# Optimization experiments

Measured on AMD Instinct MI355X. Metric: run time of the kernel, lower is better.

Reference implementation:

```python
import jax, jax.numpy as jnp
import numpy as np

D_MODEL = 2048
N_HEADS = 16
D_K = D_MODEL // N_HEADS


def setup_inputs() -> dict:
    key = jax.random.key(0)
    ks = jax.random.split(key, 9)
    s = 1.0 / np.sqrt(D_MODEL)
    def lin(k):
        kw, kb = jax.random.split(k)
        W = jax.random.uniform(kw, (D_MODEL, D_MODEL), jnp.float32, -s, s)
        b = jax.random.uniform(kb, (D_MODEL,), jnp.float32, -s, s)
        return W, b
    Wq, bq = lin(ks[0])
    Wk, bk = lin(ks[1])
    Wv, bv = lin(ks[2])
    Wo, bo = lin(ks[3])
    x = jax.random.normal(ks[4], (2, 2048, D_MODEL), jnp.float32)
    return {"x": x, "Wq": Wq, "bq": bq, "Wk": Wk, "bk": bk,
            "Wv": Wv, "bv": bv, "Wo": Wo, "bo": bo}


def _mha(x, Wq, bq, Wk, bk, Wv, bv, Wo, bo):
    B, S, _ = x.shape
    # Linear projections (torch Linear: x @ W.T + b), split into heads: b s (h d) -> b h s d
    def proj(W, b):
        y = jnp.einsum('bsm,nm->bsn', x, W) + b
        return y.reshape(B, S, N_HEADS, D_K).transpose(0, 2, 1, 3)
    q = proj(Wq, bq)
    k = proj(Wk, bk)
    v = proj(Wv, bv)
    scores = jnp.einsum('bhsd,bhtd->bhst', q, k) / jnp.sqrt(jnp.float32(D_K))
    causal = jnp.triu(jnp.ones((S, S), bool), k=1)  # True above diagonal -> masked
    scores = jnp.where(causal[None, None], -jnp.inf, scores)
    attn = jax.nn.softmax(scores, axis=-1)  # dropout p=0 (eval)
    out = jnp.einsum('bhst,bhtd->bhsd', attn, v)
    out = out.transpose(0, 2, 1, 3).reshape(B, S, D_MODEL)
    return jnp.einsum('bsm,nm->bsn', out, Wo) + bo


def reference(x, Wq, bq, Wk, bk, Wv, bv, Wo, bo):
    return _mha(x, Wq, bq, Wk, bk, Wv, bv, Wo, bo)
```

## Files before the change

kernel.cpp:

```cpp
#include <hip/hip_runtime.h>

typedef unsigned short u16;
typedef __attribute__((ext_vector_type(8))) short bf16x8;
typedef __attribute__((ext_vector_type(4))) float f32x4;
typedef __attribute__((ext_vector_type(4))) unsigned short u16x4;

__device__ __forceinline__ u16 f2bf(float f) {
  union { float f; unsigned u; } v; v.f = f;
  return (u16)((v.u + 0x7FFFu + ((v.u >> 16) & 1u)) >> 16);
}

__device__ __forceinline__ void gload16(const u16* g, u16* l) {
  __builtin_amdgcn_global_load_lds((const __attribute__((address_space(1))) void*)g,
                                   (__attribute__((address_space(3))) void*)l, 16, 0, 0);
}

__global__ __launch_bounds__(256) void k_f2bf5(
    const float* __restrict__ i0, const float* __restrict__ i1, const float* __restrict__ i2,
    const float* __restrict__ i3, const float* __restrict__ i4,
    u16* o0, u16* o1, u16* o2, u16* o3, u16* o4, int n4x, int n4w) {
  const int seg = blockIdx.y;
  const float* in = (seg == 0) ? i0 : (seg == 1) ? i1 : (seg == 2) ? i2 : (seg == 3) ? i3 : i4;
  u16* out = (seg == 0) ? o0 : (seg == 1) ? o1 : (seg == 2) ? o2 : (seg == 3) ? o3 : o4;
  const int n4 = (seg == 0) ? n4x : n4w;
  int i = blockIdx.x * 256 + threadIdx.x;
  const int stride = gridDim.x * 256;
  for (; i < n4; i += stride) {
    const float4 v = ((const float4*)in)[i];
    u16x4 o;
    o.x = f2bf(v.x); o.y = f2bf(v.y); o.z = f2bf(v.z); o.w = f2bf(v.w);
    ((u16x4*)out)[i] = o;
  }
}

template <int OUT_F32>
__global__ __launch_bounds__(256) void k_gemm_bias(
    const u16* __restrict__ A,
    const u16* __restrict__ Bt0, const u16* __restrict__ Bt1, const u16* __restrict__ Bt2,
    const float* __restrict__ b0, const float* __restrict__ b1, const float* __restrict__ b2,
    u16* __restrict__ C0, u16* __restrict__ C1, u16* __restrict__ C2,
    float* __restrict__ Cf, int M, int N, int K)
{
  const int z = blockIdx.z;
  const u16* Bt = (z == 0) ? Bt0 : (z == 1) ? Bt1 : Bt2;
  const float* bias = (z == 0) ? b0 : (z == 1) ? b1 : b2;
  u16* Cb = (z == 0) ? C0 : (z == 1) ? C1 : C2;

  __shared__ u16 As[128 * 64];
  __shared__ u16 Bs[128 * 64];
  const int tid = threadIdx.x;
  const int lane = tid & 63;
  const int wid = tid >> 6;
  const int fr = lane & 15;
  const int fg = lane >> 4;
  const int wr = wid >> 1, wc = wid & 1;
  const long row0 = (long)blockIdx.x * 128;
  const long col0 = (long)blockIdx.y * 128;

  f32x4 acc[4][4] = {};

  for (int k0 = 0; k0 < K; k0 += 64) {
    __syncthreads();
#pragma unroll
    for (int i = 0; i < 4; ++i) {
      const int chunk = (wid * 4 + i) * 64 + lane;
      const int r = chunk >> 3;
      const int c = (chunk & 7) << 3;
      gload16(A + (row0 + r) * (long)K + k0 + c, &As[(wid * 4 + i) * 512]);
      gload16(Bt + (col0 + r) * (long)K + k0 + c, &Bs[(wid * 4 + i) * 512]);
    }
    __syncthreads();

#pragma unroll
    for (int kc = 0; kc < 2; ++kc) {
      bf16x8 a[4], b[4];
#pragma unroll
      for (int i = 0; i < 4; ++i)
        a[i] = *(const bf16x8*)&As[(wr * 64 + i * 16 + fr) * 64 + kc * 32 + fg * 8];
#pragma unroll
      for (int j = 0; j < 4; ++j)
        b[j] = *(const bf16x8*)&Bs[(wc * 64 + j * 16 + fr) * 64 + kc * 32 + fg * 8];
#pragma unroll
      for (int i = 0; i < 4; ++i)
#pragma unroll
        for (int j = 0; j < 4; ++j)
          acc[i][j] = __builtin_amdgcn_mfma_f32_16x16x32_bf16(a[i], b[j], acc[i][j], 0, 0, 0);
    }
  }

#pragma unroll
  for (int j = 0; j < 4; ++j) {
    const long cN = col0 + wc * 64 + j * 16 + fr;
    const float bv = bias[cN];
#pragma unroll
    for (int i = 0; i < 4; ++i) {
      const long rM = row0 + wr * 64 + i * 16 + fg * 4;
#pragma unroll
      for (int reg = 0; reg < 4; ++reg) {
        const float v = acc[i][j][reg] + bv;
        if (OUT_F32) Cf[(rM + reg) * N + cN] = v;
        else         Cb[(rM + reg) * N + cN] = f2bf(v);
      }
    }
  }
}

__global__ __launch_bounds__(256) void k_transpose_v(const u16* __restrict__ V,
                                                     u16* __restrict__ Vt) {
  __shared__ u16 t[64][68];
  const int bh = blockIdx.z;
  const long s0 = (long)blockIdx.x * 64;
  const long d0 = (long)blockIdx.y * 64;
  const int tid = threadIdx.x;
  const long rowbase = (long)(bh >> 4) * 2048;
  const int hcol = (bh & 15) * 128;
#pragma unroll
  for (int i = 0; i < 4; ++i) {
    const int v = tid + i * 256;
    const int r = v >> 4, c4 = (v & 15) << 2;
    const u16x4 val = *(const u16x4*)&V[(rowbase + s0 + r) * 2048 + hcol + d0 + c4];
    *(u16x4*)&t[r][c4] = val;
  }
  __syncthreads();
#pragma unroll
  for (int i = 0; i < 4; ++i) {
    const int v = tid + i * 256;
    const int dr = v >> 4, s4 = (v & 15) << 2;
    u16x4 o;
    o.x = t[s4 + 0][dr]; o.y = t[s4 + 1][dr]; o.z = t[s4 + 2][dr]; o.w = t[s4 + 3][dr];
    *(u16x4*)&Vt[((long)bh * 128 + d0 + dr) * 2048 + s0 + s4] = o;
  }
}

__global__ __launch_bounds__(512) void k_flash_attn(
    const u16* __restrict__ Q, const u16* __restrict__ K, const u16* __restrict__ Vt,
    u16* __restrict__ O)
{
  __shared__ alignas(16) u16 Kt[2][8192];
  __shared__ alignas(16) u16 Vtt[2][8192];
  __shared__ alignas(16) u16 Plds[8][16][72];

  const int tid = threadIdx.x;
  const int lane = tid & 63, wid = tid >> 6;
  const int fr = lane & 15, fg = lane >> 4;

  const int L = blockIdx.x;
  const int bh = (L & 7) * 4 + ((L >> 3) & 3);
  const int bx = L >> 5;

  const long rowbase = (long)(bh >> 4) * 2048;
  const int hcol = (bh & 15) * 128;
  const u16* Kg = K + rowbase * 2048 + hcol;
  const u16* Vg = Vt + (long)bh * 128 * 2048;
  const float scale2 = 0.08838834764831845f * 1.44269504089f;

  int kR[2], kC[2], vR[2], vC[2];
#pragma unroll
  for (int i = 0; i < 2; ++i) {
    const int chunk = (wid * 2 + i) * 64 + lane;
    kR[i] = chunk >> 4;
    kC[i] = ((chunk & 15) ^ (kR[i] & 7)) << 3;
    vR[i] = chunk >> 3;
    vC[i] = ((chunk & 7) ^ (vR[i] & 7)) << 3;
  }

  const int sw = fr & 7;
  int kbase[4], vbase[2];
#pragma unroll
  for (int c = 0; c < 4; ++c) kbase[c] = fr * 128 + (((c * 4 + fg) ^ sw) << 3);
#pragma unroll
  for (int kc = 0; kc < 2; ++kc) vbase[kc] = fr * 64 + (((kc * 4 + fg) ^ sw) << 3);

  for (int pass = 0; pass < 2; ++pass) {
    const int qblk = pass ? (15 - bx) : bx;
    const int n = 2 * (qblk + 1);
    const int q_lo = qblk * 128 + wid * 16;

    bf16x8 qf[4];
#pragma unroll
    for (int c = 0; c < 4; ++c)
      qf[c] = *(const bf16x8*)&Q[(rowbase + q_lo + fr) * 2048 + hcol + c * 32 + fg * 8];

    f32x4 oacc[8] = {};
    float m_run[4], l_run[4];
#pragma unroll
    for (int r = 0; r < 4; ++r) { m_run[r] = -1e30f; l_run[r] = 0.0f; }

#pragma unroll
    for (int i = 0; i < 2; ++i) {
      gload16(Kg + (long)kR[i] * 2048 + kC[i], &Kt[0][(wid * 2 + i) * 512]);
      gload16(Vg + (long)vR[i] * 2048 + vC[i], &Vtt[0][(wid * 2 + i) * 512]);
    }

    int cur = 0;
    for (int j = 0; j < n; ++j) {
      if (j + 1 < n) {
        const long kv = (long)(j + 1) * 64;
#pragma unroll
        for (int i = 0; i < 2; ++i) {
          gload16(Kg + (kv + kR[i]) * 2048 + kC[i], &Kt[cur ^ 1][(wid * 2 + i) * 512]);
          gload16(Vg + (long)vR[i] * 2048 + kv + vC[i], &Vtt[cur ^ 1][(wid * 2 + i) * 512]);
        }
        asm volatile("s_waitcnt vmcnt(4)" ::: "memory");
      } else {
        asm volatile("s_waitcnt vmcnt(0)" ::: "memory");
      }
      __builtin_amdgcn_s_barrier();
      __builtin_amdgcn_sched_barrier(0);

      const int kvlo = j * 64;
      const bool skip = (kvlo >= q_lo + 16);
      if (!skip) {
        const bool needmask = (kvlo + 63 > q_lo);

        f32x4 st[4] = {};
        const u16* kt = Kt[cur];
#pragma unroll
        for (int t = 0; t < 4; ++t)
#pragma unroll
          for (int c = 0; c < 4; ++c) {
            const bf16x8 kf = *(const bf16x8*)&kt[kbase[c] + t * 2048];
            st[t] = __builtin_amdgcn_mfma_f32_16x16x32_bf16(qf[c], kf, st[t], 0, 0, 0);
          }

        float pmax[4] = {-1e30f, -1e30f, -1e30f, -1e30f};
        if (needmask) {
#pragma unroll
          for (int t = 0; t < 4; ++t) {
            const int kg = kvlo + t * 16 + fr;
#pragma unroll
            for (int r = 0; r < 4; ++r) {
              const int qg = q_lo + fg * 4 + r;
              const float v = (kg <= qg) ? st[t][r] * scale2 : -1e30f;
              st[t][r] = v;
              pmax[r] = fmaxf(pmax[r], v);
            }
          }
        } else {
#pragma unroll
          for (int t = 0; t < 4; ++t)
#pragma unroll
            for (int r = 0; r < 4; ++r) {
              const float v = st[t][r] * scale2;
              st[t][r] = v;
              pmax[r] = fmaxf(pmax[r], v);
            }
        }
#pragma unroll
        for (int d = 1; d < 16; d <<= 1)
#pragma unroll
          for (int r = 0; r < 4; ++r) pmax[r] = fmaxf(pmax[r], __shfl_xor(pmax[r], d));

        const int ok = (pmax[0] <= m_run[0] + 8.f) & (pmax[1] <= m_run[1] + 8.f) &
                       (pmax[2] <= m_run[2] + 8.f) & (pmax[3] <= m_run[3] + 8.f);
        if (!__all(ok)) {
#pragma unroll
          for (int r = 0; r < 4; ++r) {
            const float nm = fmaxf(m_run[r], pmax[r]);
            const float al = exp2f(m_run[r] - nm);
            l_run[r] *= al;
            m_run[r] = nm;
#pragma unroll
            for (int dt = 0; dt < 8; ++dt) oacc[dt][r] *= al;
          }
        }

        float lsum[4] = {0.f, 0.f, 0.f, 0.f};
#pragma unroll
        for (int t = 0; t < 4; ++t)
#pragma unroll
          for (int r = 0; r < 4; ++r) {
            const float p = exp2f(st[t][r] - m_run[r]);
            st[t][r] = p;
            lsum[r] += p;
          }
#pragma unroll
        for (int d = 1; d < 16; d <<= 1)
#pragma unroll
          for (int r = 0; r < 4; ++r) lsum[r] += __shfl_xor(lsum[r], d);
#pragma unroll
        for (int r = 0; r < 4; ++r) l_run[r] += lsum[r];

#pragma unroll
        for (int t = 0; t < 4; ++t)
#pragma unroll
          for (int r = 0; r < 4; ++r)
            Plds[wid][fg * 4 + r][t * 16 + fr] = f2bf(st[t][r]);
        asm volatile("s_waitcnt lgkmcnt(0)" ::: "memory");
        __builtin_amdgcn_sched_barrier(0);

        const u16* vt = Vtt[cur];
#pragma unroll
        for (int kc = 0; kc < 2; ++kc) {
          const bf16x8 pf = *(const bf16x8*)&Plds[wid][fr][kc * 32 + fg * 8];
#pragma unroll
          for (int dt = 0; dt < 8; ++dt) {
            const bf16x8 vf = *(const bf16x8*)&vt[vbase[kc] + dt * 1024];
            oacc[dt] = __builtin_amdgcn_mfma_f32_16x16x32_bf16(pf, vf, oacc[dt], 0, 0, 0);
          }
        }
      }

      asm volatile("" ::: "memory");
      __builtin_amdgcn_s_barrier();
      cur ^= 1;
    }

    float inv[4];
#pragma unroll
    for (int r = 0; r < 4; ++r) inv[r] = 1.0f / l_run[r];
#pragma unroll
    for (int dt = 0; dt < 8; ++dt)
#pragma unroll
      for (int r = 0; r < 4; ++r)
        O[(rowbase + q_lo + fg * 4 + r) * 2048 + hcol + dt * 16 + fr] = f2bf(oacc[dt][r] * inv[r]);
  }
}

extern "C" void kernel_launch(void* const* d_in, const int* in_sizes, int n_in,
                              void* d_out, int out_size, void* d_ws, size_t ws_size,
                              hipStream_t stream) {
  const float* x  = (const float*)d_in[0];
  const float* Wq = (const float*)d_in[1];
  const float* bq = (const float*)d_in[2];
  const float* Wk = (const float*)d_in[3];
  const float* bk = (const float*)d_in[4];
  const float* Wv = (const float*)d_in[5];
  const float* bv = (const float*)d_in[6];
  const float* Wo = (const float*)d_in[7];
  const float* bo = (const float*)d_in[8];
  float* out = (float*)d_out;

  const int M = 4096, N = 2048, Kd = 2048;
  char* ws = (char*)d_ws;
  const size_t SZ_X = 16777216;
  const size_t SZ_W = 8388608;
  u16* xb  = (u16*)(ws);
  u16* wqb = (u16*)(ws + SZ_X);
  u16* wkb = (u16*)(ws + SZ_X + 1 * SZ_W);
  u16* wvb = (u16*)(ws + SZ_X + 2 * SZ_W);
  u16* wob = (u16*)(ws + SZ_X + 3 * SZ_W);
  u16* Qb  = (u16*)(ws + 1 * SZ_X + 4 * SZ_W);
  u16* Kb  = (u16*)(ws + 2 * SZ_X + 4 * SZ_W);
  u16* Vb  = (u16*)(ws + 3 * SZ_X + 4 * SZ_W);
  u16* Vtb = (u16*)(ws + 4 * SZ_X + 4 * SZ_W);
  u16* Ob  = Vb;

  k_f2bf5<<<dim3(1024, 5), 256, 0, stream>>>(x, Wq, Wk, Wv, Wo,
                                             xb, wqb, wkb, wvb, wob,
                                             8388608 / 4, 4194304 / 4);

  k_gemm_bias<0><<<dim3(M / 128, N / 128, 3), 256, 0, stream>>>(
      xb, wqb, wkb, wvb, bq, bk, bv, Qb, Kb, Vb, nullptr, M, N, Kd);

  k_transpose_v<<<dim3(32, 2, 32), 256, 0, stream>>>(Vb, Vtb);

  k_flash_attn<<<256, 512, 0, stream>>>(Qb, Kb, Vtb, Ob);

  k_gemm_bias<1><<<dim3(M / 128, N / 128, 1), 256, 0, stream>>>(
      Ob, wob, wob, wob, bo, bo, bo, nullptr, nullptr, nullptr, out, M, N, Kd);
}
```

Baseline: 313.4 us.

## Replace projection GEMMs with 256x256 double-buffered swizzled LDS kernel

Replaces the 128x128 GEMM with a 512-thread kernel computing 256x256 tiles. It double-buffers LDS with global_load_lds prefetch of the next K tile and XOR-swizzles the LDS layout to avoid bank conflicts. It also interleaves MFMA phases with barriers and setprio, and remaps workgroups across XCDs for cache locality. The Q/K/V projections become one GEMM against the three contiguous weight matrices, and the bias/output pointer is picked per column segment. Larger tiles raise data reuse, at the cost of only 128 blocks for the output projection, which may underfill the GPU, plus heavy register and LDS use.

After: 322.9 us. 1.03x slower.

```diff
diff --git a/kernel.cpp b/kernel.cpp
--- a/kernel.cpp
+++ b/kernel.cpp
@@ -33,73 +33,122 @@
   }
 }
 
+#define LDA(AS, mh) do { _Pragma("unroll") \
+  for (int mi = 0; mi < 4; ++mi) { \
+    a[mi][0] = *(const bf16x8*)&(AS)[aBase + ((mh)*4+mi)*1024 + pc0]; \
+    a[mi][1] = *(const bf16x8*)&(AS)[aBase + ((mh)*4+mi)*1024 + pc1]; } } while(0)
+
+#define LDB(BS, nh) do { _Pragma("unroll") \
+  for (int ni = 0; ni < 2; ++ni) { \
+    b[nh][ni][0] = *(const bf16x8*)&(BS)[bBase + ((nh)*2+ni)*1024 + pc0]; \
+    b[nh][ni][1] = *(const bf16x8*)&(BS)[bBase + ((nh)*2+ni)*1024 + pc1]; } } while(0)
+
+#define MM(mh, nh) do { _Pragma("unroll") \
+  for (int mi = 0; mi < 4; ++mi) { _Pragma("unroll") \
+    for (int ni = 0; ni < 2; ++ni) { \
+      acc[(mh)*4+mi][(nh)*2+ni] = __builtin_amdgcn_mfma_f32_16x16x32_bf16( \
+          a[mi][0], b[nh][ni][0], acc[(mh)*4+mi][(nh)*2+ni], 0, 0, 0); \
+      acc[(mh)*4+mi][(nh)*2+ni] = __builtin_amdgcn_mfma_f32_16x16x32_bf16( \
+          a[mi][1], b[nh][ni][1], acc[(mh)*4+mi][(nh)*2+ni], 0, 0, 0); } } } while(0)
+
+#define MFMA_FENCE do { asm volatile("s_waitcnt lgkmcnt(0)" ::: "memory"); \
+  __builtin_amdgcn_sched_barrier(0); } while(0)
+
+#define KTILE(AS, BS, AN, BN_, tn) do { \
+   \
+  if ((tn) < NT) { const long kofs = (long)(tn) << 6; \
+    _Pragma("unroll") for (int i = 0; i < 4; ++i) { \
+      gload16(A  + (row0 + sRow[i]) * (long)K + kofs + sCol[i], &(AN)[(wid*4+i)*512]); \
+      gload16(Bt + (col0 + sRow[i]) * (long)K + kofs + sCol[i], &(BN_)[(wid*4+i)*512]); } } \
+  LDA(AS, 0); LDB(BS, 0); LDB(BS, 1); \
+  __builtin_amdgcn_s_barrier(); \
+  MFMA_FENCE; \
+  __builtin_amdgcn_s_setprio(1); MM(0, 0); __builtin_amdgcn_s_setprio(0); \
+  __builtin_amdgcn_s_barrier(); \
+   \
+  __builtin_amdgcn_s_setprio(1); MM(0, 1); __builtin_amdgcn_s_setprio(0); \
+  __builtin_amdgcn_s_barrier(); \
+   \
+  LDA(AS, 1); \
+  MFMA_FENCE; \
+  __builtin_amdgcn_s_setprio(1); MM(1, 0); __builtin_amdgcn_s_setprio(0); \
+  __builtin_amdgcn_s_barrier(); \
+   \
+  __builtin_amdgcn_s_setprio(1); MM(1, 1); __builtin_amdgcn_s_setprio(0); \
+  asm volatile("s_waitcnt vmcnt(0)" ::: "memory"); \
+  __builtin_amdgcn_s_barrier(); \
+} while(0)
+
 template <int OUT_F32>
-__global__ __launch_bounds__(256) void k_gemm_bias(
-    const u16* __restrict__ A,
-    const u16* __restrict__ Bt0, const u16* __restrict__ Bt1, const u16* __restrict__ Bt2,
+__global__ __launch_bounds__(512, 2) void k_gemm256(
+    const u16* __restrict__ A, const u16* __restrict__ Bt,
     const float* __restrict__ b0, const float* __restrict__ b1, const float* __restrict__ b2,
     u16* __restrict__ C0, u16* __restrict__ C1, u16* __restrict__ C2,
-    float* __restrict__ Cf, int M, int N, int K)
+    float* __restrict__ Cf, int NBM, int K)
 {
-  const int z = blockIdx.z;
-  const u16* Bt = (z == 0) ? Bt0 : (z == 1) ? Bt1 : Bt2;
-  const float* bias = (z == 0) ? b0 : (z == 1) ? b1 : b2;
-  u16* Cb = (z == 0) ? C0 : (z == 1) ? C1 : C2;
-
-  __shared__ u16 As[128 * 64];
-  __shared__ u16 Bs[128 * 64];
+  __shared__ alignas(16) u16 A0s[16384], B0s[16384], A1s[16384], B1s[16384];
+
   const int tid = threadIdx.x;
-  const int lane = tid & 63;
-  const int wid = tid >> 6;
-  const int fr = lane & 15;
-  const int fg = lane >> 4;
-  const int wr = wid >> 1, wc = wid & 1;
-  const long row0 = (long)blockIdx.x * 128;
-  const long col0 = (long)blockIdx.y * 128;
-
-  f32x4 acc[4][4] = {};
-
-  for (int k0 = 0; k0 < K; k0 += 64) {
-    __syncthreads();
-#pragma unroll
-    for (int i = 0; i < 4; ++i) {
-      const int chunk = (wid * 4 + i) * 64 + lane;
-      const int r = chunk >> 3;
-      const int c = (chunk & 7) << 3;
-      gload16(A + (row0 + r) * (long)K + k0 + c, &As[(wid * 4 + i) * 512]);
-      gload16(Bt + (col0 + r) * (long)K + k0 + c, &Bs[(wid * 4 + i) * 512]);
-    }
-    __syncthreads();
-
-#pragma unroll
-    for (int kc = 0; kc < 2; ++kc) {
-      bf16x8 a[4], b[4];
-#pragma unroll
-      for (int i = 0; i < 4; ++i)
-        a[i] = *(const bf16x8*)&As[(wr * 64 + i * 16 + fr) * 64 + kc * 32 + fg * 8];
-#pragma unroll
-      for (int j = 0; j < 4; ++j)
-        b[j] = *(const bf16x8*)&Bs[(wc * 64 + j * 16 + fr) * 64 + kc * 32 + fg * 8];
-#pragma unroll
-      for (int i = 0; i < 4; ++i)
-#pragma unroll
-        for (int j = 0; j < 4; ++j)
-          acc[i][j] = __builtin_amdgcn_mfma_f32_16x16x32_bf16(a[i], b[j], acc[i][j], 0, 0, 0);
-    }
-  }
-
-#pragma unroll
-  for (int j = 0; j < 4; ++j) {
-    const long cN = col0 + wc * 64 + j * 16 + fr;
-    const float bv = bias[cN];
-#pragma unroll
-    for (int i = 0; i < 4; ++i) {
-      const long rM = row0 + wr * 64 + i * 16 + fg * 4;
+  const int lane = tid & 63, wid = tid >> 6;
+  const int fr = lane & 15, fg = lane >> 4;
+  const int wr = wid >> 2, wc = wid & 3;
+
+  const int nblk = gridDim.x;
+  const int q = nblk >> 3, r = nblk & 7;
+  const int xcd = blockIdx.x & 7, lid = blockIdx.x >> 3;
+  const int wgid = (xcd < r ? xcd * (q + 1) : r * (q + 1) + (xcd - r) * q) + lid;
+  const int mb = wgid % NBM, nb = wgid / NBM;
+  const long row0 = (long)mb * 256;
+  const long col0 = (long)nb * 256;
+
+  int sRow[4], sCol[4];
+#pragma unroll
+  for (int i = 0; i < 4; ++i) {
+    const int s = (wid * 4 + i) * 64 + lane;
+    sRow[i] = s >> 3;
+    sCol[i] = ((s & 7) ^ ((s >> 3) & 7)) << 3;
+  }
+
+  const int sw = fr & 7;
+  const int aBase = (wr * 128 + fr) * 64;
+  const int bBase = (wc * 64 + fr) * 64;
+  const int pc0 = (fg ^ sw) << 3;
+  const int pc1 = ((4 + fg) ^ sw) << 3;
+
+  f32x4 acc[8][4] = {};
+  bf16x8 a[4][2], b[2][2][2];
+
+  const int NT = K >> 6;
+
+#pragma unroll
+  for (int i = 0; i < 4; ++i) {
+    gload16(A  + (row0 + sRow[i]) * (long)K + sCol[i], &A0s[(wid * 4 + i) * 512]);
+    gload16(Bt + (col0 + sRow[i]) * (long)K + sCol[i], &B0s[(wid * 4 + i) * 512]);
+  }
+  asm volatile("s_waitcnt vmcnt(0)" ::: "memory");
+  __builtin_amdgcn_s_barrier();
+
+  for (int t = 0; t < NT; t += 2) {
+    KTILE(A0s, B0s, A1s, B1s, t + 1);
+    KTILE(A1s, B1s, A0s, B0s, t + 2);
+  }
+
+  const int seg = (int)(col0 >> 11);
+  const long colL = col0 & 2047;
+  const float* bp = (seg == 0) ? b0 : (seg == 1) ? b1 : b2;
+  u16* Cb = (seg == 0) ? C0 : (seg == 1) ? C1 : C2;
+#pragma unroll
+  for (int n = 0; n < 4; ++n) {
+    const long cN = colL + wc * 64 + n * 16 + fr;
+    const float bv = bp[cN];
+#pragma unroll
+    for (int m = 0; m < 8; ++m) {
+      const long rM = row0 + wr * 128 + m * 16 + fg * 4;
 #pragma unroll
       for (int reg = 0; reg < 4; ++reg) {
-        const float v = acc[i][j][reg] + bv;
-        if (OUT_F32) Cf[(rM + reg) * N + cN] = v;
-        else         Cb[(rM + reg) * N + cN] = f2bf(v);
+        const float v = acc[m][n][reg] + bv;
+        if (OUT_F32) Cf[(rM + reg) * 2048 + cN] = v;
+        else         Cb[(rM + reg) * 2048 + cN] = f2bf(v);
       }
     }
   }
@@ -331,7 +380,7 @@
   const float* bo = (const float*)d_in[8];
   float* out = (float*)d_out;
 
-  const int M = 4096, N = 2048, Kd = 2048;
+  const int M = 4096, Kd = 2048;
   char* ws = (char*)d_ws;
   const size_t SZ_X = 16777216;
   const size_t SZ_W = 8388608;
@@ -350,13 +399,11 @@
                                              xb, wqb, wkb, wvb, wob,
                                              8388608 / 4, 4194304 / 4);
 
-  k_gemm_bias<0><<<dim3(M / 128, N / 128, 3), 256, 0, stream>>>(
-      xb, wqb, wkb, wvb, bq, bk, bv, Qb, Kb, Vb, nullptr, M, N, Kd);
+  k_gemm256<0><<<384, 512, 0, stream>>>(xb, wqb, bq, bk, bv, Qb, Kb, Vb, nullptr, 16, Kd);
 
   k_transpose_v<<<dim3(32, 2, 32), 256, 0, stream>>>(Vb, Vtb);
 
   k_flash_attn<<<256, 512, 0, stream>>>(Qb, Kb, Vtb, Ob);
 
-  k_gemm_bias<1><<<dim3(M / 128, N / 128, 1), 256, 0, stream>>>(
-      Ob, wob, wob, wob, bo, bo, bo, nullptr, nullptr, nullptr, out, M, N, Kd);
-}
+  k_gemm256<1><<<128, 512, 0, stream>>>(Ob, wob, bo, bo, bo, nullptr, nullptr, nullptr, out, 16, Kd);
+}
```

## Swizzle GEMM LDS tiles, remap blocks per XCD, and merge QKV weights

Applied to the files above, without the earlier changes.

The GEMM kernel now XOR-swizzles the 16-byte column chunks of each LDS row on both the global-to-LDS load and the fragment reads. This is meant to remove LDS bank conflicts on the bf16x8 reads. Block IDs are remapped so that consecutive tiles land on the same XCD, which should improve L2 reuse of A and B tiles. The three QKV weight matrices, already contiguous in the workspace, are treated as a single 6144-row B in a flat 1D grid. Sizes are now hardcoded to 2048 and a min-occupancy launch bound is added, so the kernel is specialised to this shape.

Result: faster. 280.1 us (-10.6%).

```diff
diff --git a/kernel.cpp b/kernel.cpp
--- a/kernel.cpp
+++ b/kernel.cpp
@@ -34,52 +34,64 @@
 }
 
 template <int OUT_F32>
-__global__ __launch_bounds__(256) void k_gemm_bias(
-    const u16* __restrict__ A,
-    const u16* __restrict__ Bt0, const u16* __restrict__ Bt1, const u16* __restrict__ Bt2,
+__global__ __launch_bounds__(256, 4) void k_gemm12(
+    const u16* __restrict__ A, const u16* __restrict__ Bt,
     const float* __restrict__ b0, const float* __restrict__ b1, const float* __restrict__ b2,
     u16* __restrict__ C0, u16* __restrict__ C1, u16* __restrict__ C2,
-    float* __restrict__ Cf, int M, int N, int K)
+    float* __restrict__ Cf, int NBM)
 {
-  const int z = blockIdx.z;
-  const u16* Bt = (z == 0) ? Bt0 : (z == 1) ? Bt1 : Bt2;
-  const float* bias = (z == 0) ? b0 : (z == 1) ? b1 : b2;
-  u16* Cb = (z == 0) ? C0 : (z == 1) ? C1 : C2;
-
-  __shared__ u16 As[128 * 64];
-  __shared__ u16 Bs[128 * 64];
+  __shared__ alignas(16) u16 As[8192];
+  __shared__ alignas(16) u16 Bs[8192];
+
   const int tid = threadIdx.x;
-  const int lane = tid & 63;
-  const int wid = tid >> 6;
-  const int fr = lane & 15;
-  const int fg = lane >> 4;
+  const int lane = tid & 63, wid = tid >> 6;
+  const int fr = lane & 15, fg = lane >> 4;
   const int wr = wid >> 1, wc = wid & 1;
-  const long row0 = (long)blockIdx.x * 128;
-  const long col0 = (long)blockIdx.y * 128;
+
+  const int nblk = gridDim.x;
+  const int q = nblk >> 3, r = nblk & 7;
+  const int xcd = blockIdx.x & 7, lid = blockIdx.x >> 3;
+  const int wgid = (xcd < r ? xcd * (q + 1) : r * (q + 1) + (xcd - r) * q) + lid;
+  const int mb = wgid % NBM, nb = wgid / NBM;
+  const long row0 = (long)mb * 128;
+  const long col0 = (long)nb * 128;
+
+  int sRow[4], sCol[4];
+#pragma unroll
+  for (int i = 0; i < 4; ++i) {
+    const int g = (wid * 4 + i) * 64 + lane;
+    sRow[i] = g >> 3;
+    sCol[i] = ((g & 7) ^ (sRow[i] & 7)) << 3;
+  }
+
+  const int sw = fr & 7;
+  const int aBase = (wr * 64 + fr) * 64;
+  const int bBase = (wc * 64 + fr) * 64;
+  const int pc0 = (fg ^ sw) << 3;
+  const int pc1 = ((4 + fg) ^ sw) << 3;
 
   f32x4 acc[4][4] = {};
 
-  for (int k0 = 0; k0 < K; k0 += 64) {
+#pragma unroll 1
+  for (int t = 0; t < 32; ++t) {
+    if (t) __syncthreads();
+    const long k0 = (long)t << 6;
+#pragma unroll
+    for (int i = 0; i < 4; ++i) {
+      gload16(A  + (row0 + sRow[i]) * 2048L + k0 + sCol[i], &As[(wid * 4 + i) * 512]);
+      gload16(Bt + (col0 + sRow[i]) * 2048L + k0 + sCol[i], &Bs[(wid * 4 + i) * 512]);
+    }
     __syncthreads();
-#pragma unroll
-    for (int i = 0; i < 4; ++i) {
-      const int chunk = (wid * 4 + i) * 64 + lane;
-      const int r = chunk >> 3;
-      const int c = (chunk & 7) << 3;
-      gload16(A + (row0 + r) * (long)K + k0 + c, &As[(wid * 4 + i) * 512]);
-      gload16(Bt + (col0 + r) * (long)K + k0 + c, &Bs[(wid * 4 + i) * 512]);
-    }
-    __syncthreads();
 
 #pragma unroll
     for (int kc = 0; kc < 2; ++kc) {
+      const int pc = kc ? pc1 : pc0;
       bf16x8 a[4], b[4];
 #pragma unroll
-      for (int i = 0; i < 4; ++i)
-        a[i] = *(const bf16x8*)&As[(wr * 64 + i * 16 + fr) * 64 + kc * 32 + fg * 8];
-#pragma unroll
-      for (int j = 0; j < 4; ++j)
-        b[j] = *(const bf16x8*)&Bs[(wc * 64 + j * 16 + fr) * 64 + kc * 32 + fg * 8];
+      for (int i = 0; i < 4; ++i) {
+        a[i] = *(const bf16x8*)&As[aBase + i * 1024 + pc];
+        b[i] = *(const bf16x8*)&Bs[bBase + i * 1024 + pc];
+      }
 #pragma unroll
       for (int i = 0; i < 4; ++i)
 #pragma unroll
@@ -88,18 +100,22 @@
     }
   }
 
+  const int seg = (int)(col0 >> 11);
+  const long colL = col0 & 2047;
+  const float* bp = (seg == 0) ? b0 : (seg == 1) ? b1 : b2;
+  u16* Cb = (seg == 0) ? C0 : (seg == 1) ? C1 : C2;
 #pragma unroll
   for (int j = 0; j < 4; ++j) {
-    const long cN = col0 + wc * 64 + j * 16 + fr;
-    const float bv = bias[cN];
+    const long cN = colL + wc * 64 + j * 16 + fr;
+    const float bv = bp[cN];
 #pragma unroll
     for (int i = 0; i < 4; ++i) {
       const long rM = row0 + wr * 64 + i * 16 + fg * 4;
 #pragma unroll
       for (int reg = 0; reg < 4; ++reg) {
         const float v = acc[i][j][reg] + bv;
-        if (OUT_F32) Cf[(rM + reg) * N + cN] = v;
-        else         Cb[(rM + reg) * N + cN] = f2bf(v);
+        if (OUT_F32) Cf[(rM + reg) * 2048 + cN] = v;
+        else         Cb[(rM + reg) * 2048 + cN] = f2bf(v);
       }
     }
   }
@@ -331,7 +347,6 @@
   const float* bo = (const float*)d_in[8];
   float* out = (float*)d_out;
 
-  const int M = 4096, N = 2048, Kd = 2048;
   char* ws = (char*)d_ws;
   const size_t SZ_X = 16777216;
   const size_t SZ_W = 8388608;
@@ -350,13 +365,11 @@
                                              xb, wqb, wkb, wvb, wob,
                                              8388608 / 4, 4194304 / 4);
 
-  k_gemm_bias<0><<<dim3(M / 128, N / 128, 3), 256, 0, stream>>>(
-      xb, wqb, wkb, wvb, bq, bk, bv, Qb, Kb, Vb, nullptr, M, N, Kd);
+  k_gemm12<0><<<1536, 256, 0, stream>>>(xb, wqb, bq, bk, bv, Qb, Kb, Vb, nullptr, 32);
 
   k_transpose_v<<<dim3(32, 2, 32), 256, 0, stream>>>(Vb, Vtb);
 
   k_flash_attn<<<256, 512, 0, stream>>>(Qb, Kb, Vtb, Ob);
 
-  k_gemm_bias<1><<<dim3(M / 128, N / 128, 1), 256, 0, stream>>>(
-      Ob, wob, wob, wob, bo, bo, bo, nullptr, nullptr, nullptr, out, M, N, Kd);
-}
+  k_gemm12<1><<<512, 256, 0, stream>>>(Ob, wob, bo, bo, bo, nullptr, nullptr, nullptr, out, 32);
+}
```
